# Kernel tuning notes

Measured on AMD Instinct MI355X. Metric: run time of the kernel, lower is better.

The kernel has to match this reference:

```python
import jax, jax.numpy as jnp
import numpy as np

ALPHA = 0.2  # LeakyReLU negative slope
NUM_HEADS, OUT_DIM = 8, 16
N_NODES, N_EDGES, IN_DIM = 50000, 800000, 128


def setup_inputs() -> dict:
    key = jax.random.key(0)
    k = jax.random.split(key, 6)
    return {
        "x": jax.random.normal(k[0], (N_NODES, IN_DIM), dtype=jnp.float32),
        "W1": jax.random.normal(k[1], (IN_DIM, IN_DIM), dtype=jnp.float32) * (1.414 / np.sqrt(IN_DIM)),
        "W2": jax.random.normal(k[2], (NUM_HEADS * OUT_DIM, IN_DIM), dtype=jnp.float32) * (1.414 / np.sqrt(IN_DIM)),
        "attn_l": jax.random.normal(k[3], (NUM_HEADS, OUT_DIM), dtype=jnp.float32) * 0.3,
        "attn_r": jax.random.normal(k[4], (NUM_HEADS, OUT_DIM), dtype=jnp.float32) * 0.3,
        "edge_index": jax.random.randint(k[5], (2, N_EDGES), 0, N_NODES, dtype=jnp.int64),
    }


def reference(x, W1, W2, attn_l, attn_r, edge_index):
    N = x.shape[0]
    H, D = attn_l.shape
    # fc1 -> leaky_relu -> fc2, reshape to per-head features [N, H, D]
    h2 = jax.nn.leaky_relu(x @ W1.T, ALPHA)
    ft = (h2 @ W2.T).reshape(N, H, D)
    # per-node attention halves: a1 = ft . attn_l, a2 = ft . attn_r  -> [N, H]
    a1 = jnp.einsum('nhd,hd->nh', ft, attn_l)
    a2 = jnp.einsum('nhd,hd->nh', ft, attn_r)
    src, dst = edge_index[0], edge_index[1]
    # edge attention logits [E, H]
    e = jax.nn.leaky_relu(a1[src] + a2[dst], ALPHA)
    # edge softmax normalized over incoming edges of each dst node
    emax = jax.ops.segment_max(e, dst, num_segments=N)
    ee = jnp.exp(e - emax[dst])
    esum = jax.ops.segment_sum(ee, dst, num_segments=N)
    a = ee / esum[dst]  # [E, H]
    # weighted scatter-sum aggregation: sum_{e: dst(e)=n} a_e * ft[src(e)]
    msg = ft[src] * a[:, :, None]  # [E, H, D]
    out = jax.ops.segment_sum(msg, dst, num_segments=N)  # [N, H, D]
    return out
```

## Files before the change

### kernel.cpp

```cpp
#include <hip/hip_runtime.h>

#define ALPHA 0.2f
constexpr int N = 50000;
constexpr int E = 800000;

typedef __attribute__((ext_vector_type(8))) short bf16x8;
typedef __attribute__((ext_vector_type(4))) float f32x4;

__device__ inline ushort f2bf(float v) {
  uint u = __float_as_uint(v);
  return (ushort)((u + 0x7fff + ((u >> 16) & 1)) >> 16);
}
__device__ inline float bf2f(ushort u) { return __uint_as_float(((uint)u) << 16); }

constexpr int LDX = 136;

constexpr int BN   = 128;
constexpr int NB   = (N + BN - 1) / BN;
constexpr int NBP  = 512;
constexpr int PSTR = 392;
constexpr int CHUNK = 4096;
constexpr int NBLK  = (E + CHUNK - 1) / CHUNK;
constexpr int FROWS = 32;
constexpr int FEATB = (N + FROWS - 1) / FROWS;
constexpr int SMEMB = 2 * FROWS * LDX * 2;

__global__ __launch_bounds__(256) void k1_kernel(const float* __restrict__ W1,
    const float* __restrict__ W2, ushort* __restrict__ wf1hi, ushort* __restrict__ wf1lo,
    ushort* __restrict__ wf2hi, ushort* __restrict__ wf2lo,
    const int* __restrict__ dst, int* __restrict__ partial) {
  const int bid = blockIdx.x;
  const int t = threadIdx.x;
  if (bid < NBLK) {
    __shared__ int lh[NB];
    const int e0 = bid * CHUNK, e1 = min(e0 + CHUNK, E);
    for (int i = t; i < NB; i += 256) lh[i] = 0;
    __syncthreads();
    for (int i = e0 + t; i < e1; i += 256)
      atomicAdd(&lh[((unsigned)dst[i]) >> 7], 1);
    __syncthreads();
    for (int i = t; i < NB; i += 256) partial[bid * PSTR + i] = lh[i];
    return;
  }
  int g = (bid - NBLK) * 256 + t;
  const float* W = (g < 2048) ? W1 : W2;
  ushort* whi = (g < 2048) ? wf1hi : wf2hi;
  ushort* wlo = (g < 2048) ? wf1lo : wf2lo;
  int f = g & 2047;
  int ks = f >> 9, rem = f & 511, jb = rem >> 6, l = rem & 63;
  int m = jb * 16 + (l & 15), kb = ks * 32 + (l >> 4) * 8;
#pragma unroll
  for (int q = 0; q < 2; ++q) {
    float4 v = *(const float4*)&W[m * 128 + kb + q * 4];
    ushort4 hi, lo;
    hi.x = f2bf(v.x); lo.x = f2bf(v.x - bf2f(hi.x));
    hi.y = f2bf(v.y); lo.y = f2bf(v.y - bf2f(hi.y));
    hi.z = f2bf(v.z); lo.z = f2bf(v.z - bf2f(hi.z));
    hi.w = f2bf(v.w); lo.w = f2bf(v.w - bf2f(hi.w));
    *(ushort4*)&whi[f * 8 + q * 4] = hi;
    *(ushort4*)&wlo[f * 8 + q * 4] = lo;
  }
}

__global__ __launch_bounds__(NBP) void colscan_kernel(const int* __restrict__ partial,
    int* __restrict__ bucket_base, int* __restrict__ chunk_base) {
  __shared__ int sh[NBP];
  const int t = threadIdx.x;
  int tot = 0;
  if (t < NB)
    for (int blk = 0; blk < NBLK; ++blk) tot += partial[blk * PSTR + t];
  sh[t] = (t < NB) ? tot : 0;
  __syncthreads();
  for (int off = 1; off < NBP; off <<= 1) {
    int u = (t >= off) ? sh[t - off] : 0;
    __syncthreads();
    sh[t] += u;
    __syncthreads();
  }
  if (t < NB) {
    int base = sh[t] - tot;
    bucket_base[t] = base;
    int run = base;
    for (int blk = 0; blk < NBLK; ++blk) {
      chunk_base[blk * PSTR + t] = run;
      run += partial[blk * PSTR + t];
    }
  }
  if (t == NB - 1) bucket_base[NB] = sh[t];
}

__global__ __launch_bounds__(256, 6) void featpart_kernel(
    const float* __restrict__ x,
    const ushort* __restrict__ wf1hi, const ushort* __restrict__ wf1lo,
    const ushort* __restrict__ wf2hi, const ushort* __restrict__ wf2lo,
    const float* __restrict__ attn_l, const float* __restrict__ attn_r,
    ushort* __restrict__ ft_bf, float* __restrict__ a1, float* __restrict__ a2,
    const int* __restrict__ src, const int* __restrict__ dst,
    const int* __restrict__ chunk_base, int* __restrict__ ebuf) {
  extern __shared__ char smem[];
  const int bid = blockIdx.x;
  const int tid = threadIdx.x;

  if (bid < NBLK) {
    int* curs = (int*)smem;
    const int e0 = bid * CHUNK, e1 = min(e0 + CHUNK, E);
    for (int k = tid; k < NB; k += 256) curs[k] = chunk_base[bid * PSTR + k];
    __syncthreads();
    for (int i = e0 + tid; i < e1; i += 256) {
      int s = src[i], d = dst[i];
      int pos = atomicAdd(&curs[((unsigned)d) >> 7], 1);
      ebuf[pos] = (s << 7) | (d & 127);
    }
    return;
  }

  ushort* sXhi = (ushort*)smem;
  ushort* sXlo = sXhi + FROWS * LDX;
  const int w = tid >> 6, l = tid & 63;
  const int lr = l & 15, lg4 = l >> 4;
  const int rowBase = (bid - NBLK) * FROWS;

  for (int i = tid; i < FROWS * 32; i += 256) {
    int row = i >> 5, kc = i & 31;
    int g = rowBase + row;
    float4 v = make_float4(0.f, 0.f, 0.f, 0.f);
    if (g < N) v = reinterpret_cast<const float4*>(x)[g * 32 + kc];
    ushort4 hi, lo;
    hi.x = f2bf(v.x); lo.x = f2bf(v.x - bf2f(hi.x));
    hi.y = f2bf(v.y); lo.y = f2bf(v.y - bf2f(hi.y));
    hi.z = f2bf(v.z); lo.z = f2bf(v.z - bf2f(hi.z));
    hi.w = f2bf(v.w); lo.w = f2bf(v.w - bf2f(hi.w));
    *(ushort4*)&sXhi[row * LDX + kc * 4] = hi;
    *(ushort4*)&sXlo[row * LDX + kc * 4] = lo;
  }
  __syncthreads();

  f32x4 acc[2][2];
#pragma unroll
  for (int mi = 0; mi < 2; ++mi)
#pragma unroll
    for (int jj = 0; jj < 2; ++jj) acc[mi][jj] = (f32x4){0.f, 0.f, 0.f, 0.f};

#pragma unroll
  for (int ks = 0; ks < 4; ++ks) {
    bf16x8 bh[2], bl[2], ah[2], al[2];
#pragma unroll
    for (int jj = 0; jj < 2; ++jj) {
      int off = ((ks * 8 + (2 * w + jj)) * 64 + l) * 8;
      bh[jj] = *(const bf16x8*)&wf1hi[off];
      bl[jj] = *(const bf16x8*)&wf1lo[off];
    }
#pragma unroll
    for (int mi = 0; mi < 2; ++mi) {
      int addr = (mi * 16 + lr) * LDX + ks * 32 + lg4 * 8;
      ah[mi] = *(const bf16x8*)&sXhi[addr];
      al[mi] = *(const bf16x8*)&sXlo[addr];
    }
#pragma unroll
    for (int mi = 0; mi < 2; ++mi)
#pragma unroll
      for (int jj = 0; jj < 2; ++jj) {
        acc[mi][jj] = __builtin_amdgcn_mfma_f32_16x16x32_bf16(ah[mi], bh[jj], acc[mi][jj], 0, 0, 0);
        acc[mi][jj] = __builtin_amdgcn_mfma_f32_16x16x32_bf16(ah[mi], bl[jj], acc[mi][jj], 0, 0, 0);
        acc[mi][jj] = __builtin_amdgcn_mfma_f32_16x16x32_bf16(al[mi], bh[jj], acc[mi][jj], 0, 0, 0);
      }
  }
  __syncthreads();

#pragma unroll
  for (int mi = 0; mi < 2; ++mi)
#pragma unroll
    for (int jj = 0; jj < 2; ++jj)
#pragma unroll
      for (int r = 0; r < 4; ++r) {
        float v = acc[mi][jj][r];
        v = v > 0.f ? v : ALPHA * v;
        int row = mi * 16 + lg4 * 4 + r;
        int col = w * 32 + jj * 16 + lr;
        ushort hv = f2bf(v);
        sXhi[row * LDX + col] = hv;
        sXlo[row * LDX + col] = f2bf(v - bf2f(hv));
      }
  __syncthreads();

#pragma unroll
  for (int mi = 0; mi < 2; ++mi)
#pragma unroll
    for (int jj = 0; jj < 2; ++jj) acc[mi][jj] = (f32x4){0.f, 0.f, 0.f, 0.f};

#pragma unroll
  for (int ks = 0; ks < 4; ++ks) {
    bf16x8 bh[2], bl[2], ah[2], al[2];
#pragma unroll
    for (int jj = 0; jj < 2; ++jj) {
      int off = ((ks * 8 + (2 * w + jj)) * 64 + l) * 8;
      bh[jj] = *(const bf16x8*)&wf2hi[off];
      bl[jj] = *(const bf16x8*)&wf2lo[off];
    }
#pragma unroll
    for (int mi = 0; mi < 2; ++mi) {
      int addr = (mi * 16 + lr) * LDX + ks * 32 + lg4 * 8;
      ah[mi] = *(const bf16x8*)&sXhi[addr];
      al[mi] = *(const bf16x8*)&sXlo[addr];
    }
#pragma unroll
    for (int mi = 0; mi < 2; ++mi)
#pragma unroll
      for (int jj = 0; jj < 2; ++jj) {
        acc[mi][jj] = __builtin_amdgcn_mfma_f32_16x16x32_bf16(ah[mi], bh[jj], acc[mi][jj], 0, 0, 0);
        acc[mi][jj] = __builtin_amdgcn_mfma_f32_16x16x32_bf16(ah[mi], bl[jj], acc[mi][jj], 0, 0, 0);
        acc[mi][jj] = __builtin_amdgcn_mfma_f32_16x16x32_bf16(al[mi], bh[jj], acc[mi][jj], 0, 0, 0);
      }
  }

#pragma unroll
  for (int mi = 0; mi < 2; ++mi)
#pragma unroll
    for (int jj = 0; jj < 2; ++jj) {
      int h = 2 * w + jj;
      float alv = attn_l[h * 16 + lr], arv = attn_r[h * 16 + lr];
#pragma unroll
      for (int r = 0; r < 4; ++r) {
        float v = acc[mi][jj][r];
        int grow = rowBase + mi * 16 + lg4 * 4 + r;
        bool valid = grow < N;
        if (valid) ft_bf[grow * 128 + h * 16 + lr] = f2bf(v);
        float sl = v * alv, sr = v * arv;
#pragma unroll
        for (int off = 8; off; off >>= 1) {
          sl += __shfl_xor(sl, off, 16);
          sr += __shfl_xor(sr, off, 16);
        }
        if (valid && lr == 0) { a1[grow * 8 + h] = sl; a2[grow * 8 + h] = sr; }
      }
    }
}

__global__ __launch_bounds__(256) void fine_kernel(const int* __restrict__ ebuf,
    const int* __restrict__ bucket_base, int* __restrict__ row_ptr,
    int* __restrict__ col_src) {
  __shared__ int ldeg[BN], sc[BN], curs[BN];
  const int b = blockIdx.x, t = threadIdx.x;
  const int node0 = b * BN;
  const int nloc = min(BN, N - node0);
  const int bstart = bucket_base[b], bend = bucket_base[b + 1];
  if (t < BN) ldeg[t] = 0;
  __syncthreads();
  for (int i = bstart + t; i < bend; i += 256)
    atomicAdd(&ldeg[ebuf[i] & 127], 1);
  __syncthreads();
  if (t < BN) sc[t] = ldeg[t];
  __syncthreads();
#pragma unroll
  for (int off = 1; off < BN; off <<= 1) {
    int u = (t < BN && t >= off) ? sc[t - off] : 0;
    __syncthreads();
    if (t < BN) sc[t] += u;
    __syncthreads();
  }
  if (t < nloc) {
    int base = bstart + sc[t] - ldeg[t];
    row_ptr[node0 + t] = base;
    curs[t] = base;
  }
  if (b == NB - 1 && t == 0) row_ptr[N] = bend;
  __syncthreads();
  for (int i = bstart + t; i < bend; i += 256) {
    int pr = ebuf[i];
    int pos = atomicAdd(&curs[pr & 127], 1);
    col_src[pos] = pr >> 7;
  }
}

__global__ __launch_bounds__(256) void agg_kernel(const int* __restrict__ row_ptr,
    const int* __restrict__ col_src, const ushort* __restrict__ ft_bf,
    const float* __restrict__ a1, const float* __restrict__ a2,
    float* __restrict__ out) {
  const int node = blockIdx.x * 4 + (threadIdx.x >> 6);
  if (node >= N) return;
  const int t = threadIdx.x & 63;
  const int eSlot = t >> 3;
  const int hA = t & 7;
  const int hB = t >> 3;
  const int start = row_ptr[node], end = row_ptr[node + 1];
  const float a2nA = a2[node * 8 + hA];

  float l = 0.f, acc0 = 0.f, acc1 = 0.f;
  for (int base = start; base < end; base += 8) {
    int rem = end - base; rem = rem > 8 ? 8 : rem;
    int idx = base + (eSlot < rem ? eSlot : rem - 1);
    int s = col_src[idx];
    float lg = a1[s * 8 + hA] + a2nA;
    lg = lg > 0.f ? lg : ALPHA * lg;
    float p = (eSlot < rem) ? __expf(lg) : 0.f;
#pragma unroll
    for (int e = 0; e < 8; ++e) {
      float pe = __shfl(p, e * 8 + hB);
      int se = __shfl(s, e * 8);
      ushort2 f = *(const ushort2*)&ft_bf[se * 128 + t * 2];
      l += pe;
      acc0 = fmaf(pe, bf2f(f.x), acc0);
      acc1 = fmaf(pe, bf2f(f.y), acc1);
    }
  }
  float inv = (end > start) ? 1.f / l : 0.f;
  *(float2*)&out[node * 128 + t * 2] = make_float2(acc0 * inv, acc1 * inv);
}

extern "C" void kernel_launch(void* const* d_in, const int* in_sizes, int n_in,
                              void* d_out, int out_size, void* d_ws, size_t ws_size,
                              hipStream_t stream) {
  const float* x      = (const float*)d_in[0];
  const float* W1     = (const float*)d_in[1];
  const float* W2     = (const float*)d_in[2];
  const float* attn_l = (const float*)d_in[3];
  const float* attn_r = (const float*)d_in[4];
  const int*   edge   = (const int*)d_in[5];
  const int*   src    = edge;
  const int*   dst    = edge + E;
  float* out = (float*)d_out;

  char* ws = (char*)d_ws;
  ushort* ft_bf       = (ushort*)(ws);
  float*  a1          = (float*) (ws + 12800000);
  float*  a2          = (float*) (ws + 14400000);
  int*    row_ptr     = (int*)   (ws + 16000000);
  int*    bucket_base = (int*)   (ws + 16200064);
  int*    col_src     = (int*)   (ws + 16201664);
  ushort* wf1hi       = (ushort*)(ws + 19401664);
  ushort* wf1lo       = (ushort*)(ws + 19434432);
  ushort* wf2hi       = (ushort*)(ws + 19467200);
  ushort* wf2lo       = (ushort*)(ws + 19499968);
  int*    ebuf        = (int*)   (ws + 19532736);
  int*    partial     = (int*)   (ws + 22732736);
  int*    chunk_base  = (int*)   (ws + 23040064);

  k1_kernel<<<NBLK + 16, 256, 0, stream>>>(W1, W2, wf1hi, wf1lo, wf2hi, wf2lo, dst, partial);
  colscan_kernel<<<1, NBP, 0, stream>>>(partial, bucket_base, chunk_base);
  featpart_kernel<<<NBLK + FEATB, 256, SMEMB, stream>>>(
      x, wf1hi, wf1lo, wf2hi, wf2lo, attn_l, attn_r, ft_bf, a1, a2,
      src, dst, chunk_base, ebuf);
  fine_kernel<<<NB, 256, 0, stream>>>(ebuf, bucket_base, row_ptr, col_src);
  agg_kernel<<<(N + 3) / 4, 256, 0, stream>>>(row_ptr, col_src, ft_bf, a1, a2, out);
}
```

Baseline: 98.37 us.

## Prefetch next edge batch in aggregation, wavefront-shuffle scan in fine kernel

The aggregation kernel now software-pipelines its edge loop: it loads the next 8 source indices and their attention logits while the current batch's features are accumulated, hiding the col_src and a1 gather latency. The fine kernel replaces its shared-memory Hillis-Steele scan, which needed many barriers, with wavefront shuffle scans plus a single shared total. The colscan loops also get unroll pragmas. The changes raise register pressure, and the prefetch is only worthwhile for nodes with more than 8 in-edges (about 16 on average here).

```diff
diff --git a/kernel.cpp b/kernel.cpp
--- a/kernel.cpp
+++ b/kernel.cpp
@@ -67,8 +67,10 @@
   __shared__ int sh[NBP];
   const int t = threadIdx.x;
   int tot = 0;
-  if (t < NB)
+  if (t < NB) {
+#pragma unroll 4
     for (int blk = 0; blk < NBLK; ++blk) tot += partial[blk * PSTR + t];
+  }
   sh[t] = (t < NB) ? tot : 0;
   __syncthreads();
   for (int off = 1; off < NBP; off <<= 1) {
@@ -81,6 +83,7 @@
     int base = sh[t] - tot;
     bucket_base[t] = base;
     int run = base;
+#pragma unroll 4
     for (int blk = 0; blk < NBLK; ++blk) {
       chunk_base[blk * PSTR + t] = run;
       run += partial[blk * PSTR + t];
@@ -239,7 +242,8 @@
 __global__ __launch_bounds__(256) void fine_kernel(const int* __restrict__ ebuf,
     const int* __restrict__ bucket_base, int* __restrict__ row_ptr,
     int* __restrict__ col_src) {
-  __shared__ int ldeg[BN], sc[BN], curs[BN];
+  __shared__ int ldeg[BN], curs[BN];
+  __shared__ int w0tot;
   const int b = blockIdx.x, t = threadIdx.x;
   const int node0 = b * BN;
   const int nloc = min(BN, N - node0);
@@ -249,17 +253,18 @@
   for (int i = bstart + t; i < bend; i += 256)
     atomicAdd(&ldeg[ebuf[i] & 127], 1);
   __syncthreads();
-  if (t < BN) sc[t] = ldeg[t];
-  __syncthreads();
-#pragma unroll
-  for (int off = 1; off < BN; off <<= 1) {
-    int u = (t < BN && t >= off) ? sc[t - off] : 0;
-    __syncthreads();
-    if (t < BN) sc[t] += u;
-    __syncthreads();
-  }
+  int v = (t < BN) ? ldeg[t] : 0;
+  int sc = v;
+#pragma unroll
+  for (int off = 1; off < 64; off <<= 1) {
+    int u = __shfl_up(sc, off, 64);
+    if ((t & 63) >= off) sc += u;
+  }
+  if (t == 63) w0tot = sc;
+  __syncthreads();
+  int excl = sc - v + ((t >= 64 && t < BN) ? w0tot : 0);
   if (t < nloc) {
-    int base = bstart + sc[t] - ldeg[t];
+    int base = bstart + excl;
     row_ptr[node0 + t] = base;
     curs[t] = base;
   }
@@ -286,21 +291,35 @@
   const float a2nA = a2[node * 8 + hA];
 
   float l = 0.f, acc0 = 0.f, acc1 = 0.f;
-  for (int base = start; base < end; base += 8) {
-    int rem = end - base; rem = rem > 8 ? 8 : rem;
-    int idx = base + (eSlot < rem ? eSlot : rem - 1);
-    int s = col_src[idx];
-    float lg = a1[s * 8 + hA] + a2nA;
+  if (end > start) {
+    int rem = min(end - start, 8);
+    int idx = start + (eSlot < rem ? eSlot : rem - 1);
+    int sA = col_src[idx];
+    float lg = a1[sA * 8 + hA] + a2nA;
     lg = lg > 0.f ? lg : ALPHA * lg;
-    float p = (eSlot < rem) ? __expf(lg) : 0.f;
-#pragma unroll
-    for (int e = 0; e < 8; ++e) {
-      float pe = __shfl(p, e * 8 + hB);
-      int se = __shfl(s, e * 8);
-      ushort2 f = *(const ushort2*)&ft_bf[se * 128 + t * 2];
-      l += pe;
-      acc0 = fmaf(pe, bf2f(f.x), acc0);
-      acc1 = fmaf(pe, bf2f(f.y), acc1);
+    float pA = (eSlot < rem) ? __expf(lg) : 0.f;
+
+    for (int base = start; base < end; base += 8) {
+      int nbase = base + 8;
+      int sN = 0; float pN = 0.f;
+      if (nbase < end) {
+        int rem2 = min(end - nbase, 8);
+        int idx2 = nbase + (eSlot < rem2 ? eSlot : rem2 - 1);
+        sN = col_src[idx2];
+        float lg2 = a1[sN * 8 + hA] + a2nA;
+        lg2 = lg2 > 0.f ? lg2 : ALPHA * lg2;
+        pN = (eSlot < rem2) ? __expf(lg2) : 0.f;
+      }
+#pragma unroll
+      for (int e = 0; e < 8; ++e) {
+        float pe = __shfl(pA, e * 8 + hB);
+        int se = __shfl(sA, e * 8);
+        ushort2 f = *(const ushort2*)&ft_bf[se * 128 + t * 2];
+        l += pe;
+        acc0 = fmaf(pe, bf2f(f.x), acc0);
+        acc1 = fmaf(pe, bf2f(f.y), acc1);
+      }
+      sA = sN; pA = pN;
     }
   }
   float inv = (end > start) ? 1.f / l : 0.f;
```

Measured after the change: 110.9 us. 12.7% more time.
